# Kernel optimization log

Hardware: AMD Instinct MI355X
Metric: run time of the kernel (lower is better)

## Reference

```python
import math
import jax, jax.numpy as jnp
import numpy as np

N_NODES = 50000
N_EDGES = 640000
HIDDEN = 128
NUM_RBF = 50
CUTOFF = 5.0


def setup_inputs() -> dict:
    key = jax.random.key(0)
    ks = jax.random.split(key, 12)
    h = jax.random.normal(ks[0], (N_NODES, HIDDEN), dtype=jnp.float32)
    pos = jax.random.normal(ks[1], (N_NODES, 3), dtype=jnp.float32)
    edge_index = jax.random.randint(ks[2], (2, N_EDGES), 0, N_NODES, dtype=jnp.int64)
    s_rbf = 1.0 / math.sqrt(NUM_RBF)
    s_h = 1.0 / math.sqrt(HIDDEN)
    fw1 = jax.random.normal(ks[3], (NUM_RBF, HIDDEN), dtype=jnp.float32) * s_rbf
    fb1 = jnp.zeros((HIDDEN,), dtype=jnp.float32)
    fw2 = jax.random.normal(ks[4], (HIDDEN, HIDDEN), dtype=jnp.float32) * s_h
    fb2 = jnp.zeros((HIDDEN,), dtype=jnp.float32)
    iw1 = jax.random.normal(ks[5], (HIDDEN, HIDDEN), dtype=jnp.float32) * s_h
    ib1 = jnp.zeros((HIDDEN,), dtype=jnp.float32)
    iw2 = jax.random.normal(ks[6], (HIDDEN, HIDDEN), dtype=jnp.float32) * s_h
    ib2 = jnp.zeros((HIDDEN,), dtype=jnp.float32)
    return {"h": h, "pos": pos, "edge_index": edge_index,
            "fw1": fw1, "fb1": fb1, "fw2": fw2, "fb2": fb2,
            "iw1": iw1, "ib1": ib1, "iw2": iw2, "ib2": ib2}


def reference(h, pos, edge_index, fw1, fb1, fw2, fb2, iw1, ib1, iw2, ib2):
    row, col = edge_index[0], edge_index[1]
    # pairwise distances per edge: [E]
    diff = pos[row] - pos[col]
    dist = jnp.sqrt(jnp.sum(diff * diff, axis=-1) + 1e-8)
    # Gaussian RBF expansion: [E, NUM_RBF]
    offsets = jnp.linspace(0.0, CUTOFF, NUM_RBF, dtype=jnp.float32)
    width = CUTOFF / (NUM_RBF - 1)
    rbf = jnp.exp(-0.5 * ((dist[:, None] - offsets) / width) ** 2)
    # filter net: Linear -> SiLU -> Linear, then cosine cutoff: [E, HIDDEN]
    w = jax.nn.silu(rbf @ fw1 + fb1) @ fw2 + fb2
    cut = 0.5 * (jnp.cos(jnp.pi * dist / CUTOFF) + 1.0) * (dist <= CUTOFF).astype(jnp.float32)
    w_filt = w * cut[:, None]
    # message = h[col] * filter, scatter-add to row nodes
    msg = h[col] * w_filt
    agg = jax.ops.segment_sum(msg, row, num_segments=h.shape[0])
    # interaction MLP + residual (dropout=0 / eval mode)
    out = h + (jax.nn.silu(agg @ iw1 + ib1) @ iw2 + ib2)
    return out
```

## Files before the change

### kernel.cpp

```cpp
#include <hip/hip_runtime.h>
#include <hip/hip_bf16.h>

#define HIDDEN  128
#define NUM_RBF 50
#define CUTOFF  5.0f
#define INV_WIDTH (49.0f / 5.0f)
#define OFF_STEP  (5.0f / 49.0f)
#define PI_F 3.14159265358979f

typedef __attribute__((ext_vector_type(8))) short short8;
typedef __attribute__((ext_vector_type(4))) float floatx4;

__device__ __forceinline__ unsigned short f2bf(float x) {
    union { float f; unsigned int u; } v; v.f = x;
    return (unsigned short)((v.u + 0x8000u) >> 16);
}

__device__ __forceinline__ float bfpair(unsigned int p, int hi) {
    union { unsigned int u; float f; } v;
    v.u = hi ? (p & 0xffff0000u) : (p << 16);
    return v.f;
}

__device__ __forceinline__ float silu(float x) {
    return x / (1.0f + __expf(-x));
}

__device__ __forceinline__ int swz(int row, int k) {
    return (row << 7) + (((k >> 3) ^ (row & 7)) << 3) + (k & 7);
}

__device__ __forceinline__ int swz64(int row, int k) {
    return (row << 6) + (((k >> 3) ^ (row & 7)) << 3) + (k & 7);
}

__global__ void hist_kernel(const int* __restrict__ ei, int* __restrict__ cnt,
                            int n_nodes, int n_edges)
{
    for (int e = blockIdx.x * blockDim.x + threadIdx.x; e < n_edges;
         e += gridDim.x * blockDim.x) {
        const int r = min(max(ei[e], 0), n_nodes - 1);
        atomicAdd(&cnt[r], 1);
    }
}

__global__ __launch_bounds__(256) void scan_kernel(const int* __restrict__ cnt,
                                                   int* __restrict__ cursor,
                                                   int nb)
{
    __shared__ int s[256];
    const int t = threadIdx.x;
    const int L = (nb + 255) >> 8;
    const int lo = t * L;
    const int hi = min(lo + L, nb);

    int sum = 0;
#pragma unroll 4
    for (int i = lo; i < hi; ++i) sum += cnt[i];
    s[t] = sum;
    __syncthreads();
#pragma unroll
    for (int off = 1; off < 256; off <<= 1) {
        const int u = (t >= off) ? s[t - off] : 0;
        __syncthreads();
        s[t] += u;
        __syncthreads();
    }
    int run = s[t] - sum;
#pragma unroll 4
    for (int i = lo; i < hi; ++i) {
        const int c = cnt[i];
        cursor[i] = run;
        run += c;
    }
}

__global__ void scatter_kernel(const int* __restrict__ ei,
                               const float* __restrict__ pos,
                               int* __restrict__ cursor,
                               float4* __restrict__ emeta,
                               int n_nodes, int n_edges)
{
    for (int e = blockIdx.x * blockDim.x + threadIdx.x; e < n_edges;
         e += gridDim.x * blockDim.x) {
        const int r = min(max(ei[e], 0), n_nodes - 1);
        const int c = min(max(ei[n_edges + e], 0), n_nodes - 1);
        const float dx = pos[r * 3 + 0] - pos[c * 3 + 0];
        const float dy = pos[r * 3 + 1] - pos[c * 3 + 1];
        const float dz = pos[r * 3 + 2] - pos[c * 3 + 2];
        const float dist = sqrtf(dx * dx + dy * dy + dz * dz + 1e-8f);
        const int p = atomicAdd(&cursor[r], 1);
        emeta[p] = make_float4(__int_as_float(r), __int_as_float(c), dist, 0.0f);
    }
}

template<bool SORTED>
__global__ __launch_bounds__(512, 2) void edge_mfma_kernel(
    const float* __restrict__ h,
    const float* __restrict__ pos,
    const int* __restrict__ ei,
    const float4* __restrict__ emeta,
    const float* __restrict__ fw1,
    const float* __restrict__ fb1,
    const float* __restrict__ fw2,
    const float* __restrict__ fb2,
    float* __restrict__ agg,
    int n_nodes, int n_edges)
{
    __shared__ __attribute__((aligned(16))) unsigned short fw2T[128 * 128];
    __shared__ __attribute__((aligned(16))) unsigned short fw1T[128 * 64];
    __shared__ __attribute__((aligned(16))) unsigned short tbuf[8 * 16 * 64];

    const int tid  = threadIdx.x;
    const int wave = tid >> 6;
    const int lane = tid & 63;
    const int l15  = lane & 15;
    const int quad = lane >> 4;

    for (int idx = tid; idx < HIDDEN * HIDDEN; idx += 512) {
        const int k = idx >> 7, n = idx & 127;
        fw2T[swz(n, k)] = f2bf(fw2[idx]);
    }
    for (int idx = tid; idx < HIDDEN * 64; idx += 512) {
        const int n = idx >> 6, k = idx & 63;
        const float v = (k < NUM_RBF) ? fw1[k * HIDDEN + n]
                      : (k == NUM_RBF ? fb1[n] : 0.0f);
        fw1T[swz64(n, k)] = f2bf(v);
    }

    unsigned int fb2p[4];
#pragma unroll
    for (int p = 0; p < 4; ++p) {
        fb2p[p] = ((unsigned int)f2bf(fb2[(p * 2 + 1) * 16 + l15]) << 16) |
                  (unsigned int)f2bf(fb2[(p * 2) * 16 + l15]);
    }

    __syncthreads();

    unsigned short* twave = &tbuf[wave * 16 * 64];
    const int tiles = (n_edges + 15) >> 4;

    const int nw  = gridDim.x * 8;
    const int wid = blockIdx.x * 8 + wave;
    const int qt  = tiles / nw, rmd = tiles % nw;
    const int t0  = wid * qt + min(wid, rmd);
    const int t1  = t0 + qt + (wid < rmd ? 1 : 0);

    float4 nm = make_float4(0.0f, 0.0f, 0.0f, 0.0f);
    bool   nval = false;
    if (SORTED && t0 < t1) {
        const int e = t0 * 16 + l15;
        nval = (e < n_edges);
        nm = emeta[min(e, n_edges - 1)];
    }

    int prow = -1;
    float accA = 0.0f, accB = 0.0f;

    for (int tile = t0; tile < t1; ++tile) {
        int row, col; float dist; bool valid;
        if (SORTED) {
            row = __float_as_int(nm.x); col = __float_as_int(nm.y);
            dist = nm.z; valid = nval;
            const int tn = tile + 1;
            if (tn < t1) {
                const int e = tn * 16 + l15;
                nval = (e < n_edges);
                nm = emeta[min(e, n_edges - 1)];
            }
        } else {
            const int e = tile * 16 + l15;
            valid = (e < n_edges);
            const int eidx = valid ? e : (n_edges - 1);
            row = min(max(ei[eidx], 0), n_nodes - 1);
            col = min(max(ei[n_edges + eidx], 0), n_nodes - 1);
            const float dx = pos[row * 3 + 0] - pos[col * 3 + 0];
            const float dy = pos[row * 3 + 1] - pos[col * 3 + 1];
            const float dz = pos[row * 3 + 2] - pos[col * 3 + 2];
            dist = sqrtf(dx * dx + dy * dy + dz * dz + 1e-8f);
        }
        const float cut = (valid && dist <= CUTOFF)
            ? 0.5f * (__cosf(PI_F * dist * (1.0f / CUTOFF)) + 1.0f) : 0.0f;

        int mrow[4], mcol[4]; float mcut[4];
#pragma unroll
        for (int r = 0; r < 4; ++r) {
            const int src = quad * 4 + r;
            if (!SORTED) mrow[r] = __shfl(row, src);
            mcol[r] = __shfl(col, src);
            mcut[r] = __shfl(cut, src);
        }

        unsigned int hv2[4][4];
#pragma unroll
        for (int r = 0; r < 4; ++r) {
            const float* hp = &h[(size_t)mcol[r] * HIDDEN + l15];
#pragma unroll
            for (int p = 0; p < 4; ++p) {
                const float f0 = hp[p * 32];
                const float f1 = hp[p * 32 + 16];
                hv2[r][p] = ((unsigned int)f2bf(f1) << 16) |
                            (unsigned int)f2bf(f0);
            }
        }

        short8 a1[2];
#pragma unroll
        for (int kit = 0; kit < 2; ++kit) {
            short8 f;
#pragma unroll
            for (int j = 0; j < 8; ++j) {
                const int k = kit * 32 + quad * 8 + j;
                const float x = (dist - OFF_STEP * (float)k) * INV_WIDTH;
                const float rv = (k < NUM_RBF) ? __expf(-0.5f * x * x)
                               : (k == NUM_RBF ? 1.0f : 0.0f);
                f[j] = (short)f2bf(rv);
            }
            a1[kit] = f;
        }

        short8 a2[4];
#pragma unroll
        for (int half = 0; half < 2; ++half) {
#pragma unroll
            for (int nt2 = 0; nt2 < 4; ++nt2) {
                const int nt = half * 4 + nt2;
                const short8 bA =
                    *(const short8*)&fw1T[swz64(nt * 16 + l15, quad * 8)];
                const short8 bB =
                    *(const short8*)&fw1T[swz64(nt * 16 + l15, 32 + quad * 8)];
                floatx4 c = {0.0f, 0.0f, 0.0f, 0.0f};
                c = __builtin_amdgcn_mfma_f32_16x16x32_bf16(a1[0], bA, c, 0, 0, 0);
                c = __builtin_amdgcn_mfma_f32_16x16x32_bf16(a1[1], bB, c, 0, 0, 0);
#pragma unroll
                for (int r = 0; r < 4; ++r)
                    twave[swz64(quad * 4 + r, nt2 * 16 + l15)] = f2bf(silu(c[r]));
            }
            a2[half * 2]     = *(const short8*)&twave[swz64(l15, quad * 8)];
            a2[half * 2 + 1] = *(const short8*)&twave[swz64(l15, 32 + quad * 8)];
        }

        unsigned int mask = 0;
        int r0 = 0;
        if (SORTED) {
            const int pr = __shfl(row, (l15 > 0) ? (l15 - 1) : 0);
            const unsigned long long bal =
                __ballot((l15 > 0) && (row != pr));
            mask = (unsigned int)bal & 0xFFFFu;
            r0 = __shfl(row, 0);
        }

#pragma unroll
        for (int half = 0; half < 2; ++half) {
#pragma unroll
            for (int nt2 = 0; nt2 < 4; ++nt2) {
                const int nt = half * 4 + nt2;
                const float b0 = bfpair(fb2p[nt >> 1], nt & 1);
                floatx4 c = {b0, b0, b0, b0};
#pragma unroll
                for (int kit = 0; kit < 4; ++kit) {
                    const short8 b =
                        *(const short8*)&fw2T[swz(nt * 16 + l15, kit * 32 + quad * 8)];
                    c = __builtin_amdgcn_mfma_f32_16x16x32_bf16(a2[kit], b, c, 0, 0, 0);
                }
                const int chan = nt * 16 + l15;
#pragma unroll
                for (int r = 0; r < 4; ++r) {
                    const float val = c[r] * mcut[r] * bfpair(hv2[r][nt >> 1], nt & 1);
                    if (SORTED) {
                        twave[swz64(quad * 4 + r, nt2 * 16 + l15)] = f2bf(val);
                    } else {
                        atomicAdd(&agg[mrow[r] * HIDDEN + chan], val);
                    }
                }
            }

            if (SORTED) {
                const int gchan = half * 64 + lane;
                float acc = half ? accB : accA;
                int pr = prow;
#pragma unroll
                for (int i = 0; i < 16; ++i) {
                    union { unsigned int u; float f; } v;
                    v.u = (unsigned int)twave[swz64(i, lane)] << 16;
                    const bool bnd = (i == 0) ? (r0 != pr)
                                              : ((mask >> i) & 1u);
                    if (bnd) {
                        if (pr >= 0)
                            atomicAdd(&agg[pr * HIDDEN + gchan], acc);
                        acc = 0.0f;
                        pr = __shfl(row, i);
                    }
                    acc += v.f;
                }
                if (half) { accB = acc; prow = pr; }
                else      { accA = acc; }
            }
        }
    }

    if (SORTED && prow >= 0) {
        atomicAdd(&agg[prow * HIDDEN + lane],      accA);
        atomicAdd(&agg[prow * HIDDEN + 64 + lane], accB);
    }
}

__global__ __launch_bounds__(256) void node_mfma_kernel(
    const float* __restrict__ h,
    const float* __restrict__ agg,
    const float* __restrict__ iw1,
    const float* __restrict__ ib1,
    const float* __restrict__ iw2,
    const float* __restrict__ ib2,
    float* __restrict__ out,
    int n_nodes)
{
    __shared__ __attribute__((aligned(16))) unsigned short w2T[128 * 128];
    __shared__ __attribute__((aligned(16))) unsigned short tbuf[4 * 16 * 128];

    const int tid  = threadIdx.x;
    const int wave = tid >> 6;
    const int lane = tid & 63;
    const int l15  = lane & 15;
    const int quad = lane >> 4;

    for (int idx = tid; idx < HIDDEN * HIDDEN; idx += 256) {
        const int k = idx >> 7, n = idx & 127;
        w2T[swz(n, k)] = f2bf(iw2[idx]);
    }

    short8 b1[4][8];
#pragma unroll
    for (int kit = 0; kit < 4; ++kit)
#pragma unroll
        for (int nt = 0; nt < 8; ++nt) {
            short8 f;
#pragma unroll
            for (int j = 0; j < 8; ++j) {
                const int k = kit * 32 + quad * 8 + j;
                f[j] = (short)f2bf(iw1[k * HIDDEN + nt * 16 + l15]);
            }
            b1[kit][nt] = f;
        }

    float ib1v[8], ib2v[8];
#pragma unroll
    for (int nt = 0; nt < 8; ++nt) {
        ib1v[nt] = ib1[nt * 16 + l15];
        ib2v[nt] = ib2[nt * 16 + l15];
    }

    __syncthreads();

    unsigned short* twave = &tbuf[wave * 16 * 128];
    const int tiles = (n_nodes + 15) >> 4;

    for (int tile = blockIdx.x * 4 + wave; tile < tiles; tile += gridDim.x * 4) {
        const int m0 = tile * 16;

        const int mA = min(m0 + l15, n_nodes - 1);
        short8 a1[4];
#pragma unroll
        for (int kit = 0; kit < 4; ++kit) {
            const float* p = &agg[(size_t)mA * HIDDEN + kit * 32 + quad * 8];
            short8 f;
#pragma unroll
            for (int j = 0; j < 8; ++j) f[j] = (short)f2bf(p[j]);
            a1[kit] = f;
        }

        int mo[4]; float hres[4][8];
#pragma unroll
        for (int r = 0; r < 4; ++r) {
            mo[r] = m0 + quad * 4 + r;
            const int mc = min(mo[r], n_nodes - 1);
#pragma unroll
            for (int nt = 0; nt < 8; ++nt)
                hres[r][nt] = h[(size_t)mc * HIDDEN + nt * 16 + l15];
        }

#pragma unroll
        for (int nt = 0; nt < 8; ++nt) {
            floatx4 c = {ib1v[nt], ib1v[nt], ib1v[nt], ib1v[nt]};
#pragma unroll
            for (int kit = 0; kit < 4; ++kit)
                c = __builtin_amdgcn_mfma_f32_16x16x32_bf16(a1[kit], b1[kit][nt], c, 0, 0, 0);
#pragma unroll
            for (int r = 0; r < 4; ++r)
                twave[swz(quad * 4 + r, nt * 16 + l15)] = f2bf(silu(c[r]));
        }

        short8 a2[4];
#pragma unroll
        for (int kit = 0; kit < 4; ++kit)
            a2[kit] = *(const short8*)&twave[swz(l15, kit * 32 + quad * 8)];

#pragma unroll
        for (int nt = 0; nt < 8; ++nt) {
            floatx4 c = {ib2v[nt], ib2v[nt], ib2v[nt], ib2v[nt]};
#pragma unroll
            for (int kit = 0; kit < 4; ++kit) {
                const short8 b =
                    *(const short8*)&w2T[swz(nt * 16 + l15, kit * 32 + quad * 8)];
                c = __builtin_amdgcn_mfma_f32_16x16x32_bf16(a2[kit], b, c, 0, 0, 0);
            }
            const int chan = nt * 16 + l15;
#pragma unroll
            for (int r = 0; r < 4; ++r)
                if (mo[r] < n_nodes)
                    out[(size_t)mo[r] * HIDDEN + chan] = hres[r][nt] + c[r];
        }
    }
}

extern "C" void kernel_launch(void* const* d_in, const int* in_sizes, int n_in,
                              void* d_out, int out_size, void* d_ws, size_t ws_size,
                              hipStream_t stream)
{
    const float* h   = (const float*)d_in[0];
    const float* pos = (const float*)d_in[1];
    const int*   ei  = (const int*)d_in[2];
    const float* fw1 = (const float*)d_in[3];
    const float* fb1 = (const float*)d_in[4];
    const float* fw2 = (const float*)d_in[5];
    const float* fb2 = (const float*)d_in[6];
    const float* iw1 = (const float*)d_in[7];
    const float* ib1 = (const float*)d_in[8];
    const float* iw2 = (const float*)d_in[9];
    const float* ib2 = (const float*)d_in[10];
    float* out = (float*)d_out;

    const int n_nodes = in_sizes[0] / HIDDEN;
    const int n_edges = in_sizes[2] / 2;
    const int nscan   = (n_nodes + 255) >> 8;

    const size_t need = (size_t)n_nodes * HIDDEN * sizeof(float);
    const bool use_ws = (d_ws != nullptr) && (ws_size >= need);

    const size_t moff = (((size_t)2 * n_nodes + 512) + 3) & ~(size_t)3;
    const size_t scratch_ints = moff + (size_t)4 * n_edges;
    const bool can_sort = use_ws && nscan <= 256 &&
                          ((size_t)out_size >= scratch_ints);

    if (can_sort) {
        float*  agg    = (float*)d_ws;
        int*    base   = (int*)d_out;
        int*    cnt    = base;
        int*    cursor = base + n_nodes;
        float4* emeta  = (float4*)(base + moff);

        hipMemsetAsync(cnt, 0, (size_t)n_nodes * sizeof(int), stream);
        hipMemsetAsync(agg, 0, need, stream);

        hist_kernel<<<1024, 256, 0, stream>>>(ei, cnt, n_nodes, n_edges);
        scan_kernel<<<1, 256, 0, stream>>>(cnt, cursor, n_nodes);
        scatter_kernel<<<1024, 256, 0, stream>>>(ei, pos, cursor,
                                                 emeta, n_nodes, n_edges);

        edge_mfma_kernel<true><<<256, 512, 0, stream>>>(
            h, pos, ei, emeta,
            fw1, fb1, fw2, fb2, agg, n_nodes, n_edges);

        node_mfma_kernel<<<256, 256, 0, stream>>>(h, agg, iw1, ib1, iw2, ib2,
                                                  out, n_nodes);
    } else {
        float* agg = use_ws ? (float*)d_ws : out;
        hipMemsetAsync(agg, 0, need, stream);
        edge_mfma_kernel<false><<<256, 512, 0, stream>>>(
            h, pos, ei, nullptr,
            fw1, fb1, fw2, fb2, agg, n_nodes, n_edges);
        node_mfma_kernel<<<256, 256, 0, stream>>>(h, agg, iw1, ib1, iw2, ib2,
                                                  out, n_nodes);
    }
}
```

Measured before the change: 323.9 us.

## Parallelize prefix scan across blocks and fold agg zeroing into scatter

```diff
diff --git a/kernel.cpp b/kernel.cpp
--- a/kernel.cpp
+++ b/kernel.cpp
@@ -44,20 +44,16 @@
     }
 }
 
-__global__ __launch_bounds__(256) void scan_kernel(const int* __restrict__ cnt,
-                                                   int* __restrict__ cursor,
-                                                   int nb)
+__global__ __launch_bounds__(256) void scanA_kernel(const int* __restrict__ cnt,
+                                                    int* __restrict__ cursor,
+                                                    int* __restrict__ btot,
+                                                    int nb)
 {
     __shared__ int s[256];
     const int t = threadIdx.x;
-    const int L = (nb + 255) >> 8;
-    const int lo = t * L;
-    const int hi = min(lo + L, nb);
-
-    int sum = 0;
-#pragma unroll 4
-    for (int i = lo; i < hi; ++i) sum += cnt[i];
-    s[t] = sum;
+    const int i = blockIdx.x * 256 + t;
+    const int v = (i < nb) ? cnt[i] : 0;
+    s[t] = v;
     __syncthreads();
 #pragma unroll
     for (int off = 1; off < 256; off <<= 1) {
@@ -66,30 +62,52 @@
         s[t] += u;
         __syncthreads();
     }
-    int run = s[t] - sum;
-#pragma unroll 4
-    for (int i = lo; i < hi; ++i) {
-        const int c = cnt[i];
-        cursor[i] = run;
-        run += c;
-    }
+    if (i < nb) cursor[i] = s[t] - v;
+    if (t == 255) btot[blockIdx.x] = s[255];
+}
+
+__global__ __launch_bounds__(256) void scanB_kernel(const int* __restrict__ btot,
+                                                    int* __restrict__ boff,
+                                                    int nblk)
+{
+    __shared__ int s[256];
+    const int t = threadIdx.x;
+    const int v = (t < nblk) ? btot[t] : 0;
+    s[t] = v;
+    __syncthreads();
+#pragma unroll
+    for (int off = 1; off < 256; off <<= 1) {
+        const int u = (t >= off) ? s[t - off] : 0;
+        __syncthreads();
+        s[t] += u;
+        __syncthreads();
+    }
+    if (t < nblk) boff[t] = s[t] - v;
 }
 
 __global__ void scatter_kernel(const int* __restrict__ ei,
                                const float* __restrict__ pos,
                                int* __restrict__ cursor,
+                               const int* __restrict__ boff,
                                float4* __restrict__ emeta,
+                               float4* __restrict__ aggv,
                                int n_nodes, int n_edges)
 {
-    for (int e = blockIdx.x * blockDim.x + threadIdx.x; e < n_edges;
-         e += gridDim.x * blockDim.x) {
+    const int gtid = blockIdx.x * blockDim.x + threadIdx.x;
+    const int gstr = gridDim.x * blockDim.x;
+
+    const int nv = n_nodes * 32;
+    for (int i = gtid; i < nv; i += gstr)
+        aggv[i] = make_float4(0.0f, 0.0f, 0.0f, 0.0f);
+
+    for (int e = gtid; e < n_edges; e += gstr) {
         const int r = min(max(ei[e], 0), n_nodes - 1);
         const int c = min(max(ei[n_edges + e], 0), n_nodes - 1);
         const float dx = pos[r * 3 + 0] - pos[c * 3 + 0];
         const float dy = pos[r * 3 + 1] - pos[c * 3 + 1];
         const float dz = pos[r * 3 + 2] - pos[c * 3 + 2];
         const float dist = sqrtf(dx * dx + dy * dy + dz * dz + 1e-8f);
-        const int p = atomicAdd(&cursor[r], 1);
+        const int p = boff[r >> 8] + atomicAdd(&cursor[r], 1);
         emeta[p] = make_float4(__int_as_float(r), __int_as_float(c), dist, 0.0f);
     }
 }
@@ -447,15 +465,18 @@
         int*    base   = (int*)d_out;
         int*    cnt    = base;
         int*    cursor = base + n_nodes;
+        int*    btot   = base + 2 * n_nodes;
+        int*    boff   = btot + 256;
         float4* emeta  = (float4*)(base + moff);
 
         hipMemsetAsync(cnt, 0, (size_t)n_nodes * sizeof(int), stream);
-        hipMemsetAsync(agg, 0, need, stream);
 
         hist_kernel<<<1024, 256, 0, stream>>>(ei, cnt, n_nodes, n_edges);
-        scan_kernel<<<1, 256, 0, stream>>>(cnt, cursor, n_nodes);
-        scatter_kernel<<<1024, 256, 0, stream>>>(ei, pos, cursor,
-                                                 emeta, n_nodes, n_edges);
+        scanA_kernel<<<nscan, 256, 0, stream>>>(cnt, cursor, btot, n_nodes);
+        scanB_kernel<<<1, 256, 0, stream>>>(btot, boff, nscan);
+        scatter_kernel<<<1024, 256, 0, stream>>>(ei, pos, cursor, boff,
+                                                 emeta, (float4*)agg,
+                                                 n_nodes, n_edges);
 
         edge_mfma_kernel<true><<<256, 512, 0, stream>>>(
             h, pos, ei, emeta,
```

Result: faster. 300.7 us (median of 2 runs) (-7.2%).
